# Performance work log

Measured on AMD Instinct MI355X. Metric: run time of the kernel, lower is better.

Reference implementation:

```python
import jax, jax.numpy as jnp
import numpy as np

N_NODES = 50000
N_EDGES = 800000
IN_F = 256
OUT_F = 64


def setup_inputs() -> dict:
    key = jax.random.key(0)
    k1, k2, k3, k4, k5 = jax.random.split(key, 5)
    x = jax.random.normal(k1, (N_NODES, IN_F), dtype=jnp.float32)
    # xavier-uniform-like init for weight
    limit = float(np.sqrt(6.0 / (IN_F + OUT_F)))
    weight = jax.random.uniform(k2, (IN_F, OUT_F), dtype=jnp.float32, minval=-limit, maxval=limit)
    bias = jnp.zeros((1, OUT_F), dtype=jnp.float32)
    edge_weight = jax.random.uniform(k3, (N_EDGES,), dtype=jnp.float32)
    edge_src = jax.random.randint(k4, (N_EDGES,), 0, N_NODES, dtype=jnp.int32)
    edge_dst = jax.random.randint(k5, (N_EDGES,), 0, N_NODES, dtype=jnp.int32)
    return {"x": x, "weight": weight, "bias": bias,
            "edge_weight": edge_weight, "edge_src": edge_src, "edge_dst": edge_dst}


def reference(x, weight, bias, edge_weight, edge_src, edge_dst):
    # in_features (256) > out_features (64): transform first, then propagate.
    h = x @ weight                                  # [N, out]
    # spmm with COO adjacency: out[dst] += w_e * h[src]
    msgs = h[edge_src] * edge_weight[:, None]       # [E, out]
    out = jax.ops.segment_sum(msgs, edge_dst, num_segments=x.shape[0])  # [N, out]
    return out + bias
```

## Files before the change

### kernel.cpp

```cpp
#include <hip/hip_runtime.h>
#include <hip/hip_bf16.h>

#define N_NODES 50000
#define N_EDGES 800000
#define IN_F 256
#define OUT_F 64

#define CAP 64

typedef __attribute__((ext_vector_type(8))) short short8;
typedef __attribute__((ext_vector_type(4))) float f32x4;

static __device__ __forceinline__ ushort f2bf(float v) {
    __hip_bfloat16 b = __float2bfloat16(v);
    return *(ushort*)&b;
}

__global__ __launch_bounds__(256) void gc_prep(const float* __restrict__ W,
                                               ushort* __restrict__ Wb,
                                               int* __restrict__ cnt) {
    const int g = blockIdx.x * 256 + threadIdx.x;
    if (g < N_NODES) cnt[g] = 0;
    if (g < 2048) {
        const int s = g >> 9;
        const int kk = (g >> 6) & 7;
        const int lane = g & 63;
        const int n = s * 16 + (lane & 15);
        const int kb = kk * 32 + (lane >> 4) * 8;
#pragma unroll
        for (int j = 0; j < 8; ++j)
            Wb[(size_t)g * 8 + j] = f2bf(W[(kb + j) * OUT_F + n]);
    }
}

__global__ __launch_bounds__(256) void gc_mid(const float* __restrict__ x,
                                              const ushort* __restrict__ Wb,
                                              ushort* __restrict__ h,
                                              const int* __restrict__ esrc,
                                              const int* __restrict__ edst,
                                              const float* __restrict__ ew,
                                              int* __restrict__ cnt,
                                              unsigned int* __restrict__ slots) {
    __shared__ ushort xs[32 * 264];
    const int t = threadIdx.x;
    const int bid = blockIdx.x;
    const int r3 = bid % 3;

    if (r3 == 2) {
        const int e = (bid / 3) * 1024 + t * 4;
        if (e < N_EDGES) {
            const int4 s4 = *(const int4*)(esrc + e);
            const int4 d4 = *(const int4*)(edst + e);
            const float4 w4 = *(const float4*)(ew + e);

            const int p0 = atomicAdd(&cnt[d4.x], 1);
            const int p1 = atomicAdd(&cnt[d4.y], 1);
            const int p2 = atomicAdd(&cnt[d4.z], 1);
            const int p3 = atomicAdd(&cnt[d4.w], 1);

            if (p0 < CAP)
                slots[(size_t)d4.x * CAP + p0] =
                    ((unsigned)f2bf(w4.x) << 16) | (unsigned)(s4.x & 0xFFFF);
            if (p1 < CAP)
                slots[(size_t)d4.y * CAP + p1] =
                    ((unsigned)f2bf(w4.y) << 16) | (unsigned)(s4.y & 0xFFFF);
            if (p2 < CAP)
                slots[(size_t)d4.z * CAP + p2] =
                    ((unsigned)f2bf(w4.z) << 16) | (unsigned)(s4.z & 0xFFFF);
            if (p3 < CAP)
                slots[(size_t)d4.w * CAP + p3] =
                    ((unsigned)f2bf(w4.w) << 16) | (unsigned)(s4.w & 0xFFFF);
        }
        return;
    }

    const int g = bid - bid / 3;
    const int nbase = g * 32;
    if (nbase >= N_NODES) return;

    {
#pragma unroll
        for (int i = 0; i < 8; ++i) {
            const int idx = t + i * 256;
            const int node = idx >> 6;
            const int c4 = idx & 63;
            int gnode = nbase + node;
            if (gnode >= N_NODES) gnode = N_NODES - 1;
            const float4 v = ((const float4*)x)[(size_t)gnode * 64 + c4];
            ushort4 b;
            b.x = f2bf(v.x); b.y = f2bf(v.y); b.z = f2bf(v.z); b.w = f2bf(v.w);
            *(ushort4*)&xs[node * 264 + c4 * 4] = b;
        }
    }

    const int s = t >> 6;
    const int lane = t & 63;
    const int m = lane & 15;
    const int quad = lane >> 4;

    short8 bfrag[8];
#pragma unroll
    for (int kk = 0; kk < 8; ++kk)
        bfrag[kk] = *(const short8*)(Wb + ((size_t)(s * 8 + kk) * 64 + lane) * 8);

    __syncthreads();

    f32x4 acc0 = {0.f, 0.f, 0.f, 0.f};
    f32x4 acc1 = {0.f, 0.f, 0.f, 0.f};
#pragma unroll
    for (int kk = 0; kk < 8; ++kk) {
        const short8 a0 = *(const short8*)&xs[m * 264 + kk * 32 + quad * 8];
        const short8 a1 = *(const short8*)&xs[(16 + m) * 264 + kk * 32 + quad * 8];
        acc0 = __builtin_amdgcn_mfma_f32_16x16x32_bf16(a0, bfrag[kk], acc0, 0, 0, 0);
        acc1 = __builtin_amdgcn_mfma_f32_16x16x32_bf16(a1, bfrag[kk], acc1, 0, 0, 0);
    }

#pragma unroll
    for (int r = 0; r < 4; ++r) {
        const int row0 = nbase + quad * 4 + r;
        const int row1 = row0 + 16;
        if (row0 < N_NODES) h[(size_t)row0 * OUT_F + s * 16 + m] = f2bf(acc0[r]);
        if (row1 < N_NODES) h[(size_t)row1 * OUT_F + s * 16 + m] = f2bf(acc1[r]);
    }
}

__global__ __launch_bounds__(256) void gc_gather(const ushort* __restrict__ h,
                                                 const unsigned int* __restrict__ slots,
                                                 const int* __restrict__ cnt,
                                                 const float* __restrict__ bias,
                                                 float* __restrict__ out) {
    const int wid = __builtin_amdgcn_readfirstlane(
        (int)((blockIdx.x * 256 + threadIdx.x) >> 6));
    const int f = threadIdx.x & 63;
    const int d0 = wid * 4;

    const int4 c4 = *(const int4*)(cnt + d0);
    const int dg0 = min(c4.x, CAP), dg1 = min(c4.y, CAP);
    const int dg2 = min(c4.z, CAP), dg3 = min(c4.w, CAP);
    const int mdeg = max(max(dg0, dg1), max(dg2, dg3));

    const unsigned sw0 = (f < dg0) ? slots[(size_t)(d0 + 0) * CAP + f] : 0u;
    const unsigned sw1 = (f < dg1) ? slots[(size_t)(d0 + 1) * CAP + f] : 0u;
    const unsigned sw2 = (f < dg2) ? slots[(size_t)(d0 + 2) * CAP + f] : 0u;
    const unsigned sw3 = (f < dg3) ? slots[(size_t)(d0 + 3) * CAP + f] : 0u;

    const float b = bias[f];
    float a0 = b, a1 = b, a2 = b, a3 = b;

    const ushort* __restrict__ hf = h + f;

    for (int i0 = 0; i0 < mdeg; i0 += 8) {
        unsigned hv0[8], hv1[8], hv2[8], hv3[8];
#pragma unroll
        for (int j = 0; j < 8; ++j) {
            const int l = i0 + j;
            hv0[j] = hf[(size_t)((unsigned)__builtin_amdgcn_readlane((int)sw0, l) & 0xFFFFu) * OUT_F];
            hv1[j] = hf[(size_t)((unsigned)__builtin_amdgcn_readlane((int)sw1, l) & 0xFFFFu) * OUT_F];
            hv2[j] = hf[(size_t)((unsigned)__builtin_amdgcn_readlane((int)sw2, l) & 0xFFFFu) * OUT_F];
            hv3[j] = hf[(size_t)((unsigned)__builtin_amdgcn_readlane((int)sw3, l) & 0xFFFFu) * OUT_F];
        }
#pragma unroll
        for (int j = 0; j < 8; ++j) {
            const int l = i0 + j;
            a0 += __uint_as_float((unsigned)__builtin_amdgcn_readlane((int)sw0, l) & 0xFFFF0000u)
                  * __uint_as_float(hv0[j] << 16);
            a1 += __uint_as_float((unsigned)__builtin_amdgcn_readlane((int)sw1, l) & 0xFFFF0000u)
                  * __uint_as_float(hv1[j] << 16);
            a2 += __uint_as_float((unsigned)__builtin_amdgcn_readlane((int)sw2, l) & 0xFFFF0000u)
                  * __uint_as_float(hv2[j] << 16);
            a3 += __uint_as_float((unsigned)__builtin_amdgcn_readlane((int)sw3, l) & 0xFFFF0000u)
                  * __uint_as_float(hv3[j] << 16);
        }
    }

    out[(size_t)(d0 + 0) * OUT_F + f] = a0;
    out[(size_t)(d0 + 1) * OUT_F + f] = a1;
    out[(size_t)(d0 + 2) * OUT_F + f] = a2;
    out[(size_t)(d0 + 3) * OUT_F + f] = a3;
}

extern "C" void kernel_launch(void* const* d_in, const int* in_sizes, int n_in,
                              void* d_out, int out_size, void* d_ws, size_t ws_size,
                              hipStream_t stream) {
    const float* x    = (const float*)d_in[0];
    const float* W    = (const float*)d_in[1];
    const float* bias = (const float*)d_in[2];
    const float* ew   = (const float*)d_in[3];
    const int* src    = (const int*)d_in[4];
    const int* dst    = (const int*)d_in[5];
    float* out = (float*)d_out;

    char* ws = (char*)d_ws;
    ushort* h           = (ushort*)ws;
    int* cnt            = (int*)(ws + 6400000);
    unsigned int* slots = (unsigned int*)(ws + 6600000);
    ushort* Wb          = (ushort*)(ws + 19400000);

    gc_prep<<<196, 256, 0, stream>>>(W, Wb, cnt);

    gc_mid<<<2346, 256, 0, stream>>>(x, Wb, h, src, dst, ew, cnt, slots);

    gc_gather<<<3125, 256, 0, stream>>>(h, slots, cnt, bias, out);
}
```

Baseline: 154.2 us.

## Drop weight-prep kernel and gather eight destinations per wave

Removes the separate prep kernel. The counter array is now cleared with hipMemsetAsync, and each GEMM block converts the fp32 weight fragments to bf16 itself, which removes one kernel launch and the Wb round trip. The gather kernel now handles eight destination nodes per wave instead of four, with half as many blocks, so more independent row loads are in flight. The trade-offs are redundant weight conversion in every GEMM block and higher register pressure in the gather kernel.

```diff
diff --git a/kernel.cpp b/kernel.cpp
--- a/kernel.cpp
+++ b/kernel.cpp
@@ -16,25 +16,8 @@
     return *(ushort*)&b;
 }
 
-__global__ __launch_bounds__(256) void gc_prep(const float* __restrict__ W,
-                                               ushort* __restrict__ Wb,
-                                               int* __restrict__ cnt) {
-    const int g = blockIdx.x * 256 + threadIdx.x;
-    if (g < N_NODES) cnt[g] = 0;
-    if (g < 2048) {
-        const int s = g >> 9;
-        const int kk = (g >> 6) & 7;
-        const int lane = g & 63;
-        const int n = s * 16 + (lane & 15);
-        const int kb = kk * 32 + (lane >> 4) * 8;
-#pragma unroll
-        for (int j = 0; j < 8; ++j)
-            Wb[(size_t)g * 8 + j] = f2bf(W[(kb + j) * OUT_F + n]);
-    }
-}
-
 __global__ __launch_bounds__(256) void gc_mid(const float* __restrict__ x,
-                                              const ushort* __restrict__ Wb,
+                                              const float* __restrict__ W,
                                               ushort* __restrict__ h,
                                               const int* __restrict__ esrc,
                                               const int* __restrict__ edst,
@@ -99,9 +82,17 @@
     const int quad = lane >> 4;
 
     short8 bfrag[8];
-#pragma unroll
-    for (int kk = 0; kk < 8; ++kk)
-        bfrag[kk] = *(const short8*)(Wb + ((size_t)(s * 8 + kk) * 64 + lane) * 8);
+    {
+        const float* __restrict__ wp = W + (size_t)(quad * 8) * OUT_F + s * 16 + m;
+#pragma unroll
+        for (int kk = 0; kk < 8; ++kk) {
+            short8 bf;
+#pragma unroll
+            for (int j = 0; j < 8; ++j)
+                bf[j] = (short)f2bf(wp[(size_t)(kk * 32 + j) * OUT_F]);
+            bfrag[kk] = bf;
+        }
+    }
 
     __syncthreads();
 
@@ -132,51 +123,75 @@
     const int wid = __builtin_amdgcn_readfirstlane(
         (int)((blockIdx.x * 256 + threadIdx.x) >> 6));
     const int f = threadIdx.x & 63;
-    const int d0 = wid * 4;
-
-    const int4 c4 = *(const int4*)(cnt + d0);
-    const int dg0 = min(c4.x, CAP), dg1 = min(c4.y, CAP);
-    const int dg2 = min(c4.z, CAP), dg3 = min(c4.w, CAP);
-    const int mdeg = max(max(dg0, dg1), max(dg2, dg3));
+    const int d0 = wid * 8;
+    if (d0 >= N_NODES) return;
+
+    const int4 ca = *(const int4*)(cnt + d0);
+    const int4 cb = *(const int4*)(cnt + d0 + 4);
+    const int dg0 = min(ca.x, CAP), dg1 = min(ca.y, CAP);
+    const int dg2 = min(ca.z, CAP), dg3 = min(ca.w, CAP);
+    const int dg4 = min(cb.x, CAP), dg5 = min(cb.y, CAP);
+    const int dg6 = min(cb.z, CAP), dg7 = min(cb.w, CAP);
+    const int mdeg = max(max(max(dg0, dg1), max(dg2, dg3)),
+                         max(max(dg4, dg5), max(dg6, dg7)));
 
     const unsigned sw0 = (f < dg0) ? slots[(size_t)(d0 + 0) * CAP + f] : 0u;
     const unsigned sw1 = (f < dg1) ? slots[(size_t)(d0 + 1) * CAP + f] : 0u;
     const unsigned sw2 = (f < dg2) ? slots[(size_t)(d0 + 2) * CAP + f] : 0u;
     const unsigned sw3 = (f < dg3) ? slots[(size_t)(d0 + 3) * CAP + f] : 0u;
+    const unsigned sw4 = (f < dg4) ? slots[(size_t)(d0 + 4) * CAP + f] : 0u;
+    const unsigned sw5 = (f < dg5) ? slots[(size_t)(d0 + 5) * CAP + f] : 0u;
+    const unsigned sw6 = (f < dg6) ? slots[(size_t)(d0 + 6) * CAP + f] : 0u;
+    const unsigned sw7 = (f < dg7) ? slots[(size_t)(d0 + 7) * CAP + f] : 0u;
 
     const float b = bias[f];
-    float a0 = b, a1 = b, a2 = b, a3 = b;
+    float a0 = b, a1 = b, a2 = b, a3 = b, a4 = b, a5 = b, a6 = b, a7 = b;
 
     const ushort* __restrict__ hf = h + f;
 
+#define ROWLD(sw, l) \
+    hf[(size_t)((unsigned)__builtin_amdgcn_readlane((int)(sw), (l)) & 0xFFFFu) * OUT_F]
+#define WBITS(sw, l) \
+    __uint_as_float((unsigned)__builtin_amdgcn_readlane((int)(sw), (l)) & 0xFFFF0000u)
+
     for (int i0 = 0; i0 < mdeg; i0 += 8) {
-        unsigned hv0[8], hv1[8], hv2[8], hv3[8];
+        unsigned hv0[8], hv1[8], hv2[8], hv3[8], hv4[8], hv5[8], hv6[8], hv7[8];
 #pragma unroll
         for (int j = 0; j < 8; ++j) {
             const int l = i0 + j;
-            hv0[j] = hf[(size_t)((unsigned)__builtin_amdgcn_readlane((int)sw0, l) & 0xFFFFu) * OUT_F];
-            hv1[j] = hf[(size_t)((unsigned)__builtin_amdgcn_readlane((int)sw1, l) & 0xFFFFu) * OUT_F];
-            hv2[j] = hf[(size_t)((unsigned)__builtin_amdgcn_readlane((int)sw2, l) & 0xFFFFu) * OUT_F];
-            hv3[j] = hf[(size_t)((unsigned)__builtin_amdgcn_readlane((int)sw3, l) & 0xFFFFu) * OUT_F];
+            hv0[j] = ROWLD(sw0, l);
+            hv1[j] = ROWLD(sw1, l);
+            hv2[j] = ROWLD(sw2, l);
+            hv3[j] = ROWLD(sw3, l);
+            hv4[j] = ROWLD(sw4, l);
+            hv5[j] = ROWLD(sw5, l);
+            hv6[j] = ROWLD(sw6, l);
+            hv7[j] = ROWLD(sw7, l);
         }
 #pragma unroll
         for (int j = 0; j < 8; ++j) {
             const int l = i0 + j;
-            a0 += __uint_as_float((unsigned)__builtin_amdgcn_readlane((int)sw0, l) & 0xFFFF0000u)
-                  * __uint_as_float(hv0[j] << 16);
-            a1 += __uint_as_float((unsigned)__builtin_amdgcn_readlane((int)sw1, l) & 0xFFFF0000u)
-                  * __uint_as_float(hv1[j] << 16);
-            a2 += __uint_as_float((unsigned)__builtin_amdgcn_readlane((int)sw2, l) & 0xFFFF0000u)
-                  * __uint_as_float(hv2[j] << 16);
-            a3 += __uint_as_float((unsigned)__builtin_amdgcn_readlane((int)sw3, l) & 0xFFFF0000u)
-                  * __uint_as_float(hv3[j] << 16);
-        }
-    }
+            a0 += WBITS(sw0, l) * __uint_as_float(hv0[j] << 16);
+            a1 += WBITS(sw1, l) * __uint_as_float(hv1[j] << 16);
+            a2 += WBITS(sw2, l) * __uint_as_float(hv2[j] << 16);
+            a3 += WBITS(sw3, l) * __uint_as_float(hv3[j] << 16);
+            a4 += WBITS(sw4, l) * __uint_as_float(hv4[j] << 16);
+            a5 += WBITS(sw5, l) * __uint_as_float(hv5[j] << 16);
+            a6 += WBITS(sw6, l) * __uint_as_float(hv6[j] << 16);
+            a7 += WBITS(sw7, l) * __uint_as_float(hv7[j] << 16);
+        }
+    }
+#undef ROWLD
+#undef WBITS
 
     out[(size_t)(d0 + 0) * OUT_F + f] = a0;
     out[(size_t)(d0 + 1) * OUT_F + f] = a1;
     out[(size_t)(d0 + 2) * OUT_F + f] = a2;
     out[(size_t)(d0 + 3) * OUT_F + f] = a3;
+    out[(size_t)(d0 + 4) * OUT_F + f] = a4;
+    out[(size_t)(d0 + 5) * OUT_F + f] = a5;
+    out[(size_t)(d0 + 6) * OUT_F + f] = a6;
+    out[(size_t)(d0 + 7) * OUT_F + f] = a7;
 }
 
 extern "C" void kernel_launch(void* const* d_in, const int* in_sizes, int n_in,
@@ -194,11 +209,10 @@
     ushort* h           = (ushort*)ws;
     int* cnt            = (int*)(ws + 6400000);
     unsigned int* slots = (unsigned int*)(ws + 6600000);
-    ushort* Wb          = (ushort*)(ws + 19400000);
-
-    gc_prep<<<196, 256, 0, stream>>>(W, Wb, cnt);
-
-    gc_mid<<<2346, 256, 0, stream>>>(x, Wb, h, src, dst, ew, cnt, slots);
-
-    gc_gather<<<3125, 256, 0, stream>>>(h, slots, cnt, bias, out);
-}
+
+    hipMemsetAsync(cnt, 0, N_NODES * sizeof(int), stream);
+
+    gc_mid<<<2346, 256, 0, stream>>>(x, W, h, src, dst, ew, cnt, slots);
+
+    gc_gather<<<1563, 256, 0, stream>>>(h, slots, cnt, bias, out);
+}
```

After: 155.9 us. About the same (+1.1%).
